# Performance work log

Hardware: AMD Instinct MI355X
Metric: run time of the kernel (lower is better)

The kernel has to match this reference:

```python
import jax, jax.numpy as jnp
import numpy as np

B, L, D, H = 2, 2048, 512, 8
HS = D // H          # head_size = 64
BLOCK = 2048         # block_size
EPS = 1e-5


def setup_inputs() -> dict:
    key = jax.random.key(0)
    ks = jax.random.split(key, 8)
    s = 0.02
    x = jax.random.normal(ks[0], (B, L, D), jnp.float32)
    mask = jnp.triu(jnp.ones((1, 1, L, L), bool), k=1)  # causal: True above diag
    wq = jax.random.normal(ks[1], (D, D), jnp.float32) * s
    wk = jax.random.normal(ks[2], (D, D), jnp.float32) * s
    wv = jax.random.normal(ks[3], (D, D), jnp.float32) * s
    wo = jax.random.normal(ks[4], (D, D), jnp.float32) * s
    Er = jax.random.normal(ks[5], (H, BLOCK, HS), jnp.float32)
    bq = jnp.zeros((D,), jnp.float32)
    bk = jnp.zeros((D,), jnp.float32)
    bv = jnp.zeros((D,), jnp.float32)
    bo = jnp.zeros((D,), jnp.float32)
    ln_g = jnp.ones((D,), jnp.float32)
    ln_b = jnp.zeros((D,), jnp.float32)
    return dict(x=x, mask=mask, ln_g=ln_g, ln_b=ln_b, wq=wq, bq=bq,
                wk=wk, bk=bk, wv=wv, bv=bv, wo=wo, bo=bo, Er=Er)


def _skew(qe):
    # qe: [B, H, L, L] -> pad last dim on the left, reshape trick, drop first row
    padded = jnp.pad(qe, ((0, 0), (0, 0), (0, 0), (1, 0)))
    b, h, l, l1 = padded.shape
    return padded.reshape(b, h, l1, l)[:, :, 1:, :]


def reference(x, mask, ln_g, ln_b, wq, bq, wk, bk, wv, bv, wo, bo, Er):
    l = x.shape[1]
    # LayerNorm
    mu = jnp.mean(x, axis=-1, keepdims=True)
    var = jnp.mean((x - mu) ** 2, axis=-1, keepdims=True)
    hn = (x - mu) / jnp.sqrt(var + EPS) * ln_g + ln_b
    # QKV: [B, H, L, HS]
    q = (hn @ wq.T + bq).reshape(-1, l, H, HS).transpose(0, 2, 1, 3)
    k = (hn @ wk.T + bk).reshape(-1, l, H, HS).transpose(0, 2, 1, 3)
    v = (hn @ wv.T + bv).reshape(-1, l, H, HS).transpose(0, 2, 1, 3)
    # relative position bias via skew
    Ers = Er[:, BLOCK - l:, :]                       # [H, l, HS]
    QEr = jnp.einsum('bhld,hmd->bhlm', q, Ers)       # [B, H, L, L]
    SRel = _skew(QEr)
    # scaled dot-product scores
    w = jnp.einsum('bhld,bhmd->bhlm', q, k) * (HS ** -0.5)
    w = jnp.where(mask, -jnp.inf, w)
    SRel = jnp.where(mask, -jnp.inf, SRel)
    w = jax.nn.softmax(w + SRel, axis=-1)            # dropout omitted (eval mode)
    out = jnp.einsum('bhlm,bhmd->bhld', w, v)
    out = out.transpose(0, 2, 1, 3).reshape(-1, l, D)
    return out @ wo.T + bo
```

## Files before the change

kernel.cpp:

```cpp
#include <hip/hip_runtime.h>

#define LSEQ 2048
#define DIM 512
#define NH 8
#define HS 64

typedef __attribute__((ext_vector_type(8))) short short8;
typedef __attribute__((ext_vector_type(4))) float f32x4;

__device__ inline unsigned short f2bf(float f) {
  union { float f; unsigned u; } a; a.f = f;
  unsigned r = a.u + 0x7FFFu + ((a.u >> 16) & 1u);
  return (unsigned short)(r >> 16);
}
__device__ inline float bf2f(unsigned short h) {
  union { unsigned u; float f; } a; a.u = ((unsigned)h) << 16;
  return a.f;
}
__device__ inline unsigned cvtpk(float lo, float hi) {
  unsigned r;
  asm("v_cvt_pk_bf16_f32 %0, %1, %2" : "=v"(r) : "v"(lo), "v"(hi));
  return r;
}

__device__ inline f32x4 mfma_bf16(short8 a, short8 b, f32x4 c) {
  return __builtin_amdgcn_mfma_f32_16x16x32_bf16(a, b, c, 0, 0, 0);
}

__device__ inline short8 ld8(const unsigned short* p) {
  return *reinterpret_cast<const short8*>(p);
}

#define GLLDS(SRC, DST) __builtin_amdgcn_global_load_lds( \
    (const __attribute__((address_space(1))) void*)(SRC), \
    (__attribute__((address_space(3))) void*)(DST), 16, 0, 0)

__device__ inline int frag_idx(int row, int d) {
  return (((row >> 4) * 2 + (d >> 5)) << 9) + (((row & 15) + ((d >> 3) & 3) * 16) << 3) + (d & 7);
}

__global__ __launch_bounds__(256) void cvt_all_kernel(
    const float* __restrict__ wq, const float* __restrict__ wk,
    const float* __restrict__ wv, const float* __restrict__ wo,
    const float* __restrict__ Er,
    unsigned short* __restrict__ wqb, unsigned short* __restrict__ wkb,
    unsigned short* __restrict__ wvb, unsigned short* __restrict__ wob,
    unsigned short* __restrict__ erb) {
  int b = blockIdx.x;
  if (b < 1024) {
    const float* src; unsigned short* dst; int off;
    if (b < 256)       { src = wq; dst = wqb; off = b; }
    else if (b < 512)  { src = wk; dst = wkb; off = b - 256; }
    else if (b < 768)  { src = wv; dst = wvb; off = b - 512; }
    else               { src = wo; dst = wob; off = b - 768; }
    int i = (off * 256 + threadIdx.x) * 4;
    float4 v = *reinterpret_cast<const float4*>(src + i);
    unsigned lo = (unsigned)f2bf(v.x) | ((unsigned)f2bf(v.y) << 16);
    unsigned hi = (unsigned)f2bf(v.z) | ((unsigned)f2bf(v.w) << 16);
    uint2 pk; pk.x = lo; pk.y = hi;
    *reinterpret_cast<uint2*>(dst + i) = pk;
  } else {
    const float scl = 1.4426950408889634f;
    int i = ((b - 1024) * 256 + threadIdx.x) * 4;
    int hh = i >> 17;
    int rem = i & ((1 << 17) - 1);
    int er = rem >> 6, d = rem & 63;
    float4 v = *reinterpret_cast<const float4*>(Er + i);
    unsigned lo = (unsigned)f2bf(v.x * scl) | ((unsigned)f2bf(v.y * scl) << 16);
    unsigned hi = (unsigned)f2bf(v.z * scl) | ((unsigned)f2bf(v.w * scl) << 16);
    uint2 pk; pk.x = lo; pk.y = hi;
    unsigned short* dst = erb + (size_t)hh * LSEQ * HS + frag_idx(er, d);
    *reinterpret_cast<uint2*>(dst) = pk;
  }
}

__global__ __launch_bounds__(256) void ln_kernel(const float* __restrict__ x,
    const float* __restrict__ g, const float* __restrict__ bta,
    unsigned short* __restrict__ hn) {
  int lane = threadIdx.x & 63, w = threadIdx.x >> 6;
  int row = blockIdx.x * 4 + w;
  const float4* xr = reinterpret_cast<const float4*>(x + (size_t)row * DIM);
  float4 a = xr[2 * lane], c = xr[2 * lane + 1];
  float s = a.x + a.y + a.z + a.w + c.x + c.y + c.z + c.w;
  float sq = a.x * a.x + a.y * a.y + a.z * a.z + a.w * a.w +
             c.x * c.x + c.y * c.y + c.z * c.z + c.w * c.w;
#pragma unroll
  for (int off = 1; off < 64; off <<= 1) {
    s += __shfl_xor(s, off);
    sq += __shfl_xor(sq, off);
  }
  float mu = s * (1.f / DIM);
  float var = sq * (1.f / DIM) - mu * mu;
  float rstd = rsqrtf(var + 1e-5f);
  float4 g0 = reinterpret_cast<const float4*>(g)[2 * lane];
  float4 g1 = reinterpret_cast<const float4*>(g)[2 * lane + 1];
  float4 b0 = reinterpret_cast<const float4*>(bta)[2 * lane];
  float4 b1 = reinterpret_cast<const float4*>(bta)[2 * lane + 1];
  uint4 o;
  o.x = (unsigned)f2bf((a.x - mu) * rstd * g0.x + b0.x) |
        ((unsigned)f2bf((a.y - mu) * rstd * g0.y + b0.y) << 16);
  o.y = (unsigned)f2bf((a.z - mu) * rstd * g0.z + b0.z) |
        ((unsigned)f2bf((a.w - mu) * rstd * g0.w + b0.w) << 16);
  o.z = (unsigned)f2bf((c.x - mu) * rstd * g1.x + b1.x) |
        ((unsigned)f2bf((c.y - mu) * rstd * g1.y + b1.y) << 16);
  o.w = (unsigned)f2bf((c.z - mu) * rstd * g1.z + b1.z) |
        ((unsigned)f2bf((c.w - mu) * rstd * g1.w + b1.w) << 16);
  reinterpret_cast<uint4*>(hn)[(size_t)row * 64 + lane] = o;
}

__global__ __launch_bounds__(256, 3) void qkv_kernel(const unsigned short* __restrict__ hn,
    const unsigned short* __restrict__ wqb, const unsigned short* __restrict__ wkb,
    const unsigned short* __restrict__ wvb,
    const float* __restrict__ bq, const float* __restrict__ bk, const float* __restrict__ bv,
    unsigned short* __restrict__ qo, unsigned short* __restrict__ ko,
    unsigned short* __restrict__ vT) {
  __shared__ unsigned short As[3][128 * 32];
  __shared__ unsigned short Bs[3][128 * 32];
  int tid = threadIdx.x, lane = tid & 63, w = tid >> 6;
  int mcol = lane & 15, grp = lane >> 4;
  int l4 = lane >> 2, lql = lane & 3;
  int bid = blockIdx.x;
  int mat = bid >> 7;
  int rem = bid & 127;
  int m0 = (rem >> 2) << 7;
  int n0 = (rem & 3) << 7;
  const unsigned short* W = (mat == 0) ? wqb : (mat == 1) ? wkb : wvb;
  const float* bias = (mat == 0) ? bq : (mat == 1) ? bk : bv;
  float scl = (mat == 1) ? 0.18033688011112042f : 1.f;
  int wr = w >> 1, wc = w & 1;

  f32x4 acc[4][4];
#pragma unroll
  for (int i = 0; i < 4; ++i)
#pragma unroll
    for (int j = 0; j < 4; ++j) acc[i][j] = (f32x4){0.f, 0.f, 0.f, 0.f};

#pragma unroll
  for (int j = 0; j < 2; ++j) {
    int row = 32 * w + 16 * j + l4;
    GLLDS(hn + (size_t)(m0 + row) * DIM + lql * 8, &As[0][(32 * w + 16 * j) * 32]);
    GLLDS(W + (size_t)(n0 + row) * DIM + lql * 8, &Bs[0][(32 * w + 16 * j) * 32]);
  }
  for (int kk = 0; kk < 16; ++kk) {
    int buf = kk % 3;
    if (kk < 15) {
      int nbuf = (kk + 1) % 3;
      int k0 = (kk + 1) * 32;
#pragma unroll
      for (int j = 0; j < 2; ++j) {
        int row = 32 * w + 16 * j + l4;
        GLLDS(hn + (size_t)(m0 + row) * DIM + k0 + lql * 8, &As[nbuf][(32 * w + 16 * j) * 32]);
        GLLDS(W + (size_t)(n0 + row) * DIM + k0 + lql * 8, &Bs[nbuf][(32 * w + 16 * j) * 32]);
      }
      asm volatile("s_waitcnt vmcnt(4)\n\ts_barrier" ::: "memory");
    } else {
      asm volatile("s_waitcnt vmcnt(0)\n\ts_barrier" ::: "memory");
    }
    const unsigned short* AL = As[buf];
    const unsigned short* BL = Bs[buf];
    short8 af[4], bf[4];
#pragma unroll
    for (int f = 0; f < 4; ++f) {
      af[f] = ld8(&AL[(wr * 64 + f * 16 + mcol) * 32 + grp * 8]);
      bf[f] = ld8(&BL[(wc * 64 + f * 16 + mcol) * 32 + grp * 8]);
    }
#pragma unroll
    for (int fi = 0; fi < 4; ++fi)
#pragma unroll
      for (int fj = 0; fj < 4; ++fj)
        acc[fi][fj] = mfma_bf16(af[fi], bf[fj], acc[fi][fj]);
  }
#pragma unroll
  for (int fj = 0; fj < 4; ++fj) {
    int n = n0 + wc * 64 + fj * 16 + mcol;
    int hh = n >> 6, d = n & 63;
    float bsv = bias[n];
#pragma unroll
    for (int fi = 0; fi < 4; ++fi) {
#pragma unroll
      for (int r = 0; r < 4; ++r) {
        int m = m0 + wr * 64 + fi * 16 + 4 * grp + r;
        float val = (acc[fi][fj][r] + bsv) * scl;
        int b = m >> 11, l = m & (LSEQ - 1);
        unsigned short hv = f2bf(val);
        size_t base = (size_t)(b * NH + hh) * HS * LSEQ;
        if (mat == 2) {
          int idx = (((l >> 5) * 4 + (d >> 4)) * 64 + ((l >> 3) & 3) * 16 + (d & 15)) * 8 + (l & 7);
          vT[base + idx] = hv;
        } else if (mat == 1) {
          ko[base + frag_idx(l, d)] = hv;
        } else {
          qo[((size_t)(b * NH + hh) * LSEQ + l) * HS + d] = hv;
        }
      }
    }
  }
}

__global__ __launch_bounds__(256, 3) void attn_kernel(const unsigned short* __restrict__ q,
    const unsigned short* __restrict__ k, const unsigned short* __restrict__ vT,
    const unsigned short* __restrict__ erb, char* __restrict__ partials) {
  __shared__ float Uall[4][16 * 84];
  int tid = threadIdx.x, lane = tid & 63, w = tid >> 6;
  int mcol = lane & 15, grp = lane >> 4;
  float* U = Uall[w];

  int bid = blockIdx.x;
  int xcd = bid & 7, s = bid >> 3;
  int hi2 = (s >= 80) ? 1 : 0;
  int bh = xcd + 8 * hi2;
  int ub = 79 - (s - 80 * hi2);
  int gp = (ub < 8) ? 0 : (ub < 24) ? 1 : (ub < 48) ? 2 : 3;
  int st0 = (gp == 0) ? 0 : (gp == 1) ? 8 : (gp == 2) ? 24 : 48;
  int idx = ub - st0;
  int tq = idx / (gp + 1);
  int cc = idx - tq * (gp + 1);
  int t64 = 8 * gp + tq;
  int qi0 = t64 << 6;
  int c0 = cc << 9;
  int kend = min(c0 + 512, qi0 + 64);
  int nkb = (kend - c0 + 63) >> 6;
  int h = bh & 7;

  const unsigned short* Qb = q + (size_t)bh * LSEQ * HS;
  const unsigned short* Kb = k + (size_t)bh * LSEQ * HS;
  const unsigned short* Vb = vT + (size_t)bh * HS * LSEQ;
  const unsigned short* Eb = erb + (size_t)h * LSEQ * HS;

  int qi0w = qi0 + 16 * w;
  short8 qf0 = ld8(Qb + (size_t)(qi0w + mcol) * HS + 8 * grp);
  short8 qf1 = ld8(Qb + (size_t)(qi0w + mcol) * HS + 32 + 8 * grp);

  f32x4 o[4];
#pragma unroll
  for (int i = 0; i < 4; ++i) o[i] = (f32x4){0.f, 0.f, 0.f, 0.f};
  float lacc = 0.f;
  int srcA = mcol | ((grp & 1) << 5);
  int srcB = srcA + 16;
  bool hi = (grp >= 2);
  int loff = lane * 8;

  for (int kb = 0; kb < nkb; ++kb) {
    int kj0 = c0 + (kb << 6);
    int E0w = 2032 - qi0w + kj0;
    short8 kf[8];
#pragma unroll
    for (int t = 0; t < 4; ++t) {
      int blk = ((kj0 >> 4) + t) * 2;
      kf[2 * t]     = ld8(Kb + (size_t)blk * 512 + loff);
      kf[2 * t + 1] = ld8(Kb + (size_t)(blk + 1) * 512 + loff);
    }
    short8 vf[8];
#pragma unroll
    for (int s2 = 0; s2 < 2; ++s2)
#pragma unroll
      for (int dt = 0; dt < 4; ++dt)
        vf[s2 * 4 + dt] = ld8(Vb + (size_t)(((kj0 >> 5) + s2) * 4 + dt) * 512 + loff);
#pragma unroll
    for (int jt = 0; jt < 5; ++jt) {
      int g = (E0w >> 4) + jt;
      if (g > 127) g = 127;
      short8 ef0 = ld8(Eb + (size_t)(g * 2) * 512 + loff);
      short8 ef1 = ld8(Eb + (size_t)(g * 2 + 1) * 512 + loff);
      f32x4 uu = (f32x4){0.f, 0.f, 0.f, 0.f};
      uu = mfma_bf16(ef0, qf0, uu);
      uu = mfma_bf16(ef1, qf1, uu);
      *reinterpret_cast<f32x4*>(&U[mcol * 84 + 16 * jt + 4 * grp]) = uu;
    }
    f32x4 stv[4];
#pragma unroll
    for (int t = 0; t < 4; ++t) {
      f32x4 a_ = (f32x4){0.f, 0.f, 0.f, 0.f};
      a_ = mfma_bf16(kf[2 * t], qf0, a_);
      a_ = mfma_bf16(kf[2 * t + 1], qf1, a_);
      stv[t] = a_;
    }
    float lt[4][4];
    bool anymask = (kj0 + 63) > qi0w;
    if (anymask) {
#pragma unroll
      for (int t = 0; t < 4; ++t) {
        const float* up = &U[mcol * 84 + 16 * t + 4 * grp - mcol + 15];
#pragma unroll
        for (int r = 0; r < 4; ++r) {
          int n = 16 * t + 4 * grp + r;
          float val = stv[t][r] + up[r];
          val = (kj0 + n > qi0w + mcol) ? -1e30f : val;
          float p_ = exp2f(val);
          lt[t][r] = p_;
          lacc += p_;
        }
      }
    } else {
#pragma unroll
      for (int t = 0; t < 4; ++t) {
        const float* up = &U[mcol * 84 + 16 * t + 4 * grp - mcol + 15];
#pragma unroll
        for (int r = 0; r < 4; ++r) {
          float p_ = exp2f(stv[t][r] + up[r]);
          lt[t][r] = p_;
          lacc += p_;
        }
      }
    }
    unsigned w0[4], w1[4];
#pragma unroll
    for (int t = 0; t < 4; ++t) {
      w0[t] = cvtpk(lt[t][0], lt[t][1]);
      w1[t] = cvtpk(lt[t][2], lt[t][3]);
    }
#pragma unroll
    for (int s2 = 0; s2 < 2; ++s2) {
      unsigned y0a = (unsigned)__shfl((int)w0[2 * s2], srcA);
      unsigned y0b = (unsigned)__shfl((int)w0[2 * s2 + 1], srcA);
      unsigned y1a = (unsigned)__shfl((int)w1[2 * s2], srcA);
      unsigned y1b = (unsigned)__shfl((int)w1[2 * s2 + 1], srcA);
      unsigned y2a = (unsigned)__shfl((int)w0[2 * s2], srcB);
      unsigned y2b = (unsigned)__shfl((int)w0[2 * s2 + 1], srcB);
      unsigned y3a = (unsigned)__shfl((int)w1[2 * s2], srcB);
      unsigned y3b = (unsigned)__shfl((int)w1[2 * s2 + 1], srcB);
      union { unsigned u4[4]; short8 s8; } pu;
      pu.u4[0] = hi ? y0b : y0a;
      pu.u4[1] = hi ? y1b : y1a;
      pu.u4[2] = hi ? y2b : y2a;
      pu.u4[3] = hi ? y3b : y3a;
#pragma unroll
      for (int dt = 0; dt < 4; ++dt)
        o[dt] = mfma_bf16(vf[s2 * 4 + dt], pu.s8, o[dt]);
    }
  }

  float lsum = lacc;
  lsum += __shfl_xor(lsum, 16);
  lsum += __shfl_xor(lsum, 32);

  int pid = bh * 320 + ub * 4 + w;
  char* pb = partials + (size_t)pid * 2176;
  unsigned* Ob = (unsigned*)pb;
#pragma unroll
  for (int dt = 0; dt < 4; ++dt) {
    Ob[mcol * 32 + dt * 8 + grp * 2]     = cvtpk(o[dt][0], o[dt][1]);
    Ob[mcol * 32 + dt * 8 + grp * 2 + 1] = cvtpk(o[dt][2], o[dt][3]);
  }
  if (grp == 0) {
    ((float*)(pb + 2112))[mcol] = lsum;
  }
}

__global__ __launch_bounds__(256) void merge_kernel(const char* __restrict__ partials,
    unsigned short* __restrict__ attT) {
  int lane = threadIdx.x & 63, widx = threadIdx.x >> 6;
  int bid = blockIdx.x;
  int xcd = bid & 7, q_ = bid >> 3;
  int hi2 = (q_ >= 32) ? 1 : 0;
  int bh = xcd + 8 * hi2;
  int i = (q_ - 32 * hi2) * 4 + widx;
  int t64 = i >> 2, w = i & 3;
  int gp = t64 >> 3, tq = t64 & 7;
  int st0 = (gp == 0) ? 0 : (gp == 1) ? 8 : (gp == 2) ? 24 : 48;
  int nch = gp + 1;
  int row = lane >> 2, d0 = (lane & 3) << 4;
  float acc[16];
#pragma unroll
  for (int j = 0; j < 16; ++j) acc[j] = 0.f;
  float lsum = 0.f;
  for (int c = 0; c < nch; ++c) {
    int pid = bh * 320 + (st0 + tq * nch + c) * 4 + w;
    const char* pb = partials + (size_t)pid * 2176;
    lsum += ((const float*)(pb + 2112))[row];
    short8 v0 = *reinterpret_cast<const short8*>(pb + row * 128 + d0 * 2);
    short8 v1 = *reinterpret_cast<const short8*>(pb + row * 128 + d0 * 2 + 16);
#pragma unroll
    for (int j = 0; j < 8; ++j) {
      acc[j]     += bf2f((unsigned short)v0[j]);
      acc[8 + j] += bf2f((unsigned short)v1[j]);
    }
  }
  float inv = 1.f / lsum;
  int b = bh >> 3, h = bh & 7;
  unsigned short* dst = attT + ((size_t)(b * LSEQ) + i * 16 + row) * DIM + h * HS + d0;
  union { unsigned short us[16]; short8 s8[2]; } ou;
#pragma unroll
  for (int j = 0; j < 16; ++j) ou.us[j] = f2bf(acc[j] * inv);
  *reinterpret_cast<short8*>(dst) = ou.s8[0];
  *reinterpret_cast<short8*>(dst + 8) = ou.s8[1];
}

__global__ __launch_bounds__(256, 3) void out_kernel(const unsigned short* __restrict__ attT,
    const unsigned short* __restrict__ wob, const float* __restrict__ bo,
    float* __restrict__ out) {
  __shared__ unsigned short As[3][128 * 32];
  __shared__ unsigned short Bs[3][64 * 32];
  int tid = threadIdx.x, lane = tid & 63, w = tid >> 6;
  int mcol = lane & 15, grp = lane >> 4;
  int l4 = lane >> 2, lql = lane & 3;
  int bid = blockIdx.x;
  int m0 = (bid >> 3) << 7;
  int n0 = (bid & 7) << 6;
  int wr = w >> 1, wc = w & 1;

  f32x4 acc[4][2];
#pragma unroll
  for (int i = 0; i < 4; ++i)
#pragma unroll
    for (int j = 0; j < 2; ++j) acc[i][j] = (f32x4){0.f, 0.f, 0.f, 0.f};

#pragma unroll
  for (int j = 0; j < 2; ++j) {
    int row = 32 * w + 16 * j + l4;
    GLLDS(attT + (size_t)(m0 + row) * DIM + lql * 8, &As[0][(32 * w + 16 * j) * 32]);
  }
  {
    int row = 16 * w + l4;
    GLLDS(wob + (size_t)(n0 + row) * DIM + lql * 8, &Bs[0][(16 * w) * 32]);
  }
  for (int kk = 0; kk < 16; ++kk) {
    int buf = kk % 3;
    if (kk < 15) {
      int nbuf = (kk + 1) % 3;
      int k0 = (kk + 1) * 32;
#pragma unroll
      for (int j = 0; j < 2; ++j) {
        int row = 32 * w + 16 * j + l4;
        GLLDS(attT + (size_t)(m0 + row) * DIM + k0 + lql * 8, &As[nbuf][(32 * w + 16 * j) * 32]);
      }
      {
        int row = 16 * w + l4;
        GLLDS(wob + (size_t)(n0 + row) * DIM + k0 + lql * 8, &Bs[nbuf][(16 * w) * 32]);
      }
      asm volatile("s_waitcnt vmcnt(3)\n\ts_barrier" ::: "memory");
    } else {
      asm volatile("s_waitcnt vmcnt(0)\n\ts_barrier" ::: "memory");
    }
    const unsigned short* AL = As[buf];
    const unsigned short* BL = Bs[buf];
    short8 af[4], bf[2];
#pragma unroll
    for (int f = 0; f < 4; ++f)
      af[f] = ld8(&AL[(wr * 64 + f * 16 + mcol) * 32 + grp * 8]);
#pragma unroll
    for (int f = 0; f < 2; ++f)
      bf[f] = ld8(&BL[(wc * 32 + f * 16 + mcol) * 32 + grp * 8]);
#pragma unroll
    for (int fi = 0; fi < 4; ++fi)
#pragma unroll
      for (int fj = 0; fj < 2; ++fj)
        acc[fi][fj] = mfma_bf16(af[fi], bf[fj], acc[fi][fj]);
  }
#pragma unroll
  for (int fj = 0; fj < 2; ++fj) {
    int n = n0 + wc * 32 + fj * 16 + mcol;
    float bsv = bo[n];
#pragma unroll
    for (int fi = 0; fi < 4; ++fi) {
#pragma unroll
      for (int r = 0; r < 4; ++r) {
        int m = m0 + wr * 64 + fi * 16 + 4 * grp + r;
        out[(size_t)m * DIM + n] = acc[fi][fj][r] + bsv;
      }
    }
  }
}

extern "C" void kernel_launch(void* const* d_in, const int* in_sizes, int n_in,
                              void* d_out, int out_size, void* d_ws, size_t ws_size,
                              hipStream_t stream) {
  const float* x    = (const float*)d_in[0];
  const float* ln_g = (const float*)d_in[2];
  const float* ln_b = (const float*)d_in[3];
  const float* wq   = (const float*)d_in[4];
  const float* bq   = (const float*)d_in[5];
  const float* wk   = (const float*)d_in[6];
  const float* bk   = (const float*)d_in[7];
  const float* wv   = (const float*)d_in[8];
  const float* bv   = (const float*)d_in[9];
  const float* wo   = (const float*)d_in[10];
  const float* bo   = (const float*)d_in[11];
  const float* Er   = (const float*)d_in[12];
  float* out = (float*)d_out;

  char* ws = (char*)d_ws;
  unsigned short* hn   = (unsigned short*)(ws);
  unsigned short* qb   = (unsigned short*)(ws + (4u << 20));
  unsigned short* kb   = (unsigned short*)(ws + (8u << 20));
  unsigned short* vT   = (unsigned short*)(ws + (12u << 20));
  unsigned short* erb  = (unsigned short*)(ws + (16u << 20));
  unsigned short* attT = (unsigned short*)(ws + (18u << 20));
  unsigned short* wqb  = (unsigned short*)(ws + (22u << 20));
  unsigned short* wkb  = wqb + 512 * 512;
  unsigned short* wvb  = wkb + 512 * 512;
  unsigned short* wob  = wvb + 512 * 512;
  char* partials       = ws + (24u << 20);

  cvt_all_kernel<<<2048, 256, 0, stream>>>(wq, wk, wv, wo, Er, wqb, wkb, wvb, wob, erb);
  ln_kernel<<<1024, 256, 0, stream>>>(x, ln_g, ln_b, hn);
  qkv_kernel<<<384, 256, 0, stream>>>(hn, wqb, wkb, wvb, bq, bk, bv, qb, kb, vT);
  attn_kernel<<<1280, 256, 0, stream>>>(qb, kb, vT, erb, partials);
  merge_kernel<<<512, 256, 0, stream>>>(partials, attT);
  out_kernel<<<256, 256, 0, stream>>>(attT, wob, bo, out);
}
```

Before: 83.45 us.

## Give each attention wave 32 query rows to reuse K, V and Er fragments

Each wave now owns two 16-row query groups (32 rows) instead of one, so the K, V and relative-position Er fragments it loads are reused across both groups. Work units become 32-row tiles per wave, which halves the attention grid and changes the partials layout and merge indexing to match. The exp2f call is replaced by the raw v_exp_f32 instruction. This costs more registers per wave (doubled accumulators and score tiles) and more LDS, which may lower occupancy, and the larger tiles give coarser load balance across the causal triangle.

Measured after the change: 76.57 us. -8.3%, faster.

```diff
diff --git a/kernel.cpp b/kernel.cpp
--- a/kernel.cpp
+++ b/kernel.cpp
@@ -20,6 +20,11 @@
 __device__ inline unsigned cvtpk(float lo, float hi) {
   unsigned r;
   asm("v_cvt_pk_bf16_f32 %0, %1, %2" : "=v"(r) : "v"(lo), "v"(hi));
+  return r;
+}
+__device__ inline float fexp2(float x) {
+  float r;
+  asm("v_exp_f32 %0, %1" : "=v"(r) : "v"(x));
   return r;
 }
 
@@ -200,25 +205,25 @@
 __global__ __launch_bounds__(256, 3) void attn_kernel(const unsigned short* __restrict__ q,
     const unsigned short* __restrict__ k, const unsigned short* __restrict__ vT,
     const unsigned short* __restrict__ erb, char* __restrict__ partials) {
-  __shared__ float Uall[4][16 * 84];
+  __shared__ float Uall[4][32 * 100];
   int tid = threadIdx.x, lane = tid & 63, w = tid >> 6;
   int mcol = lane & 15, grp = lane >> 4;
   float* U = Uall[w];
 
   int bid = blockIdx.x;
   int xcd = bid & 7, s = bid >> 3;
-  int hi2 = (s >= 80) ? 1 : 0;
+  int hi2 = (s >= 40) ? 1 : 0;
   int bh = xcd + 8 * hi2;
-  int ub = 79 - (s - 80 * hi2);
-  int gp = (ub < 8) ? 0 : (ub < 24) ? 1 : (ub < 48) ? 2 : 3;
-  int st0 = (gp == 0) ? 0 : (gp == 1) ? 8 : (gp == 2) ? 24 : 48;
-  int idx = ub - st0;
-  int tq = idx / (gp + 1);
-  int cc = idx - tq * (gp + 1);
-  int t64 = 8 * gp + tq;
-  int qi0 = t64 << 6;
+  int bu = s - 40 * hi2;
+  int ubp = 159 - (bu * 4 + w);
+  int T, cc;
+  if (ubp < 16)      { T = ubp; cc = 0; }
+  else if (ubp < 48) { int idx = ubp - 16; T = 16 + (idx >> 1); cc = idx & 1; }
+  else if (ubp < 96) { int idx = ubp - 48; int t3 = idx / 3; T = 32 + t3; cc = idx - 3 * t3; }
+  else               { int idx = ubp - 96; T = 48 + (idx >> 2); cc = idx & 3; }
+  int qi0w = T << 5;
   int c0 = cc << 9;
-  int kend = min(c0 + 512, qi0 + 64);
+  int kend = min(c0 + 512, qi0w + 32);
   int nkb = (kend - c0 + 63) >> 6;
   int h = bh & 7;
 
@@ -227,14 +232,19 @@
   const unsigned short* Vb = vT + (size_t)bh * HS * LSEQ;
   const unsigned short* Eb = erb + (size_t)h * LSEQ * HS;
 
-  int qi0w = qi0 + 16 * w;
-  short8 qf0 = ld8(Qb + (size_t)(qi0w + mcol) * HS + 8 * grp);
-  short8 qf1 = ld8(Qb + (size_t)(qi0w + mcol) * HS + 32 + 8 * grp);
-
-  f32x4 o[4];
-#pragma unroll
-  for (int i = 0; i < 4; ++i) o[i] = (f32x4){0.f, 0.f, 0.f, 0.f};
-  float lacc = 0.f;
+  short8 qf[2][2];
+#pragma unroll
+  for (int mg = 0; mg < 2; ++mg) {
+    qf[mg][0] = ld8(Qb + (size_t)(qi0w + 16 * mg + mcol) * HS + 8 * grp);
+    qf[mg][1] = ld8(Qb + (size_t)(qi0w + 16 * mg + mcol) * HS + 32 + 8 * grp);
+  }
+
+  f32x4 o[2][4];
+#pragma unroll
+  for (int mg = 0; mg < 2; ++mg)
+#pragma unroll
+    for (int i = 0; i < 4; ++i) o[mg][i] = (f32x4){0.f, 0.f, 0.f, 0.f};
+  float la0 = 0.f, la1 = 0.f;
   int srcA = mcol | ((grp & 1) << 5);
   int srcB = srcA + 16;
   bool hi = (grp >= 2);
@@ -242,7 +252,27 @@
 
   for (int kb = 0; kb < nkb; ++kb) {
     int kj0 = c0 + (kb << 6);
-    int E0w = 2032 - qi0w + kj0;
+    int E0 = 2016 - qi0w + kj0;
+    int g0 = E0 >> 4;
+    short8 ef[12];
+#pragma unroll
+    for (int jt = 0; jt < 6; ++jt) {
+      int gg = g0 + jt;
+      if (gg > 127) gg = 127;
+      ef[2 * jt]     = ld8(Eb + (size_t)(gg * 2) * 512 + loff);
+      ef[2 * jt + 1] = ld8(Eb + (size_t)(gg * 2 + 1) * 512 + loff);
+    }
+#pragma unroll
+    for (int jt = 0; jt < 6; ++jt) {
+      f32x4 u0 = (f32x4){0.f, 0.f, 0.f, 0.f};
+      u0 = mfma_bf16(ef[2 * jt], qf[0][0], u0);
+      u0 = mfma_bf16(ef[2 * jt + 1], qf[0][1], u0);
+      f32x4 u1 = (f32x4){0.f, 0.f, 0.f, 0.f};
+      u1 = mfma_bf16(ef[2 * jt], qf[1][0], u1);
+      u1 = mfma_bf16(ef[2 * jt + 1], qf[1][1], u1);
+      *reinterpret_cast<f32x4*>(&U[mcol * 100 + 16 * jt + 4 * grp]) = u0;
+      *reinterpret_cast<f32x4*>(&U[(mcol + 16) * 100 + 16 * jt + 4 * grp]) = u1;
+    }
     short8 kf[8];
 #pragma unroll
     for (int t = 0; t < 4; ++t) {
@@ -250,6 +280,48 @@
       kf[2 * t]     = ld8(Kb + (size_t)blk * 512 + loff);
       kf[2 * t + 1] = ld8(Kb + (size_t)(blk + 1) * 512 + loff);
     }
+    f32x4 stv[2][4];
+#pragma unroll
+    for (int mg = 0; mg < 2; ++mg)
+#pragma unroll
+      for (int t = 0; t < 4; ++t) {
+        f32x4 a_ = (f32x4){0.f, 0.f, 0.f, 0.f};
+        a_ = mfma_bf16(kf[2 * t], qf[mg][0], a_);
+        a_ = mfma_bf16(kf[2 * t + 1], qf[mg][1], a_);
+        stv[mg][t] = a_;
+      }
+    float lt[2][4][4];
+#pragma unroll
+    for (int mg = 0; mg < 2; ++mg) {
+      int m = mcol + 16 * mg;
+      bool am = (kj0 + 63) > (qi0w + 16 * mg);
+      if (am) {
+#pragma unroll
+        for (int t = 0; t < 4; ++t) {
+          const float* up = &U[m * 100 + 16 * t + 4 * grp - m + 31];
+#pragma unroll
+          for (int r = 0; r < 4; ++r) {
+            int n = 16 * t + 4 * grp + r;
+            float val = stv[mg][t][r] + up[r];
+            val = (kj0 + n > qi0w + m) ? -1e30f : val;
+            float p_ = fexp2(val);
+            lt[mg][t][r] = p_;
+            if (mg == 0) la0 += p_; else la1 += p_;
+          }
+        }
+      } else {
+#pragma unroll
+        for (int t = 0; t < 4; ++t) {
+          const float* up = &U[m * 100 + 16 * t + 4 * grp - m + 31];
+#pragma unroll
+          for (int r = 0; r < 4; ++r) {
+            float p_ = fexp2(stv[mg][t][r] + up[r]);
+            lt[mg][t][r] = p_;
+            if (mg == 0) la0 += p_; else la1 += p_;
+          }
+        }
+      }
+    }
     short8 vf[8];
 #pragma unroll
     for (int s2 = 0; s2 < 2; ++s2)
@@ -257,133 +329,94 @@
       for (int dt = 0; dt < 4; ++dt)
         vf[s2 * 4 + dt] = ld8(Vb + (size_t)(((kj0 >> 5) + s2) * 4 + dt) * 512 + loff);
 #pragma unroll
-    for (int jt = 0; jt < 5; ++jt) {
-      int g = (E0w >> 4) + jt;
-      if (g > 127) g = 127;
-      short8 ef0 = ld8(Eb + (size_t)(g * 2) * 512 + loff);
-      short8 ef1 = ld8(Eb + (size_t)(g * 2 + 1) * 512 + loff);
-      f32x4 uu = (f32x4){0.f, 0.f, 0.f, 0.f};
-      uu = mfma_bf16(ef0, qf0, uu);
-      uu = mfma_bf16(ef1, qf1, uu);
-      *reinterpret_cast<f32x4*>(&U[mcol * 84 + 16 * jt + 4 * grp]) = uu;
-    }
-    f32x4 stv[4];
-#pragma unroll
-    for (int t = 0; t < 4; ++t) {
-      f32x4 a_ = (f32x4){0.f, 0.f, 0.f, 0.f};
-      a_ = mfma_bf16(kf[2 * t], qf0, a_);
-      a_ = mfma_bf16(kf[2 * t + 1], qf1, a_);
-      stv[t] = a_;
-    }
-    float lt[4][4];
-    bool anymask = (kj0 + 63) > qi0w;
-    if (anymask) {
+    for (int mg = 0; mg < 2; ++mg) {
+      unsigned w0[4], w1[4];
 #pragma unroll
       for (int t = 0; t < 4; ++t) {
-        const float* up = &U[mcol * 84 + 16 * t + 4 * grp - mcol + 15];
-#pragma unroll
-        for (int r = 0; r < 4; ++r) {
-          int n = 16 * t + 4 * grp + r;
-          float val = stv[t][r] + up[r];
-          val = (kj0 + n > qi0w + mcol) ? -1e30f : val;
-          float p_ = exp2f(val);
-          lt[t][r] = p_;
-          lacc += p_;
-        }
-      }
-    } else {
-#pragma unroll
-      for (int t = 0; t < 4; ++t) {
-        const float* up = &U[mcol * 84 + 16 * t + 4 * grp - mcol + 15];
-#pragma unroll
-        for (int r = 0; r < 4; ++r) {
-          float p_ = exp2f(stv[t][r] + up[r]);
-          lt[t][r] = p_;
-          lacc += p_;
-        }
-      }
-    }
-    unsigned w0[4], w1[4];
-#pragma unroll
-    for (int t = 0; t < 4; ++t) {
-      w0[t] = cvtpk(lt[t][0], lt[t][1]);
-      w1[t] = cvtpk(lt[t][2], lt[t][3]);
-    }
-#pragma unroll
-    for (int s2 = 0; s2 < 2; ++s2) {
-      unsigned y0a = (unsigned)__shfl((int)w0[2 * s2], srcA);
-      unsigned y0b = (unsigned)__shfl((int)w0[2 * s2 + 1], srcA);
-      unsigned y1a = (unsigned)__shfl((int)w1[2 * s2], srcA);
-      unsigned y1b = (unsigned)__shfl((int)w1[2 * s2 + 1], srcA);
-      unsigned y2a = (unsigned)__shfl((int)w0[2 * s2], srcB);
-      unsigned y2b = (unsigned)__shfl((int)w0[2 * s2 + 1], srcB);
-      unsigned y3a = (unsigned)__shfl((int)w1[2 * s2], srcB);
-      unsigned y3b = (unsigned)__shfl((int)w1[2 * s2 + 1], srcB);
-      union { unsigned u4[4]; short8 s8; } pu;
-      pu.u4[0] = hi ? y0b : y0a;
-      pu.u4[1] = hi ? y1b : y1a;
-      pu.u4[2] = hi ? y2b : y2a;
-      pu.u4[3] = hi ? y3b : y3a;
-#pragma unroll
-      for (int dt = 0; dt < 4; ++dt)
-        o[dt] = mfma_bf16(vf[s2 * 4 + dt], pu.s8, o[dt]);
-    }
-  }
-
-  float lsum = lacc;
-  lsum += __shfl_xor(lsum, 16);
-  lsum += __shfl_xor(lsum, 32);
-
-  int pid = bh * 320 + ub * 4 + w;
-  char* pb = partials + (size_t)pid * 2176;
+        w0[t] = cvtpk(lt[mg][t][0], lt[mg][t][1]);
+        w1[t] = cvtpk(lt[mg][t][2], lt[mg][t][3]);
+      }
+#pragma unroll
+      for (int s2 = 0; s2 < 2; ++s2) {
+        unsigned y0a = (unsigned)__shfl((int)w0[2 * s2], srcA);
+        unsigned y0b = (unsigned)__shfl((int)w0[2 * s2 + 1], srcA);
+        unsigned y1a = (unsigned)__shfl((int)w1[2 * s2], srcA);
+        unsigned y1b = (unsigned)__shfl((int)w1[2 * s2 + 1], srcA);
+        unsigned y2a = (unsigned)__shfl((int)w0[2 * s2], srcB);
+        unsigned y2b = (unsigned)__shfl((int)w0[2 * s2 + 1], srcB);
+        unsigned y3a = (unsigned)__shfl((int)w1[2 * s2], srcB);
+        unsigned y3b = (unsigned)__shfl((int)w1[2 * s2 + 1], srcB);
+        union { unsigned u4[4]; short8 s8; } pu;
+        pu.u4[0] = hi ? y0b : y0a;
+        pu.u4[1] = hi ? y1b : y1a;
+        pu.u4[2] = hi ? y2b : y2a;
+        pu.u4[3] = hi ? y3b : y3a;
+#pragma unroll
+        for (int dt = 0; dt < 4; ++dt)
+          o[mg][dt] = mfma_bf16(vf[s2 * 4 + dt], pu.s8, o[mg][dt]);
+      }
+    }
+  }
+
+  la0 += __shfl_xor(la0, 16);
+  la0 += __shfl_xor(la0, 32);
+  la1 += __shfl_xor(la1, 16);
+  la1 += __shfl_xor(la1, 32);
+
+  int pid = bh * 160 + ubp;
+  char* pb = partials + (size_t)pid * 4224;
   unsigned* Ob = (unsigned*)pb;
 #pragma unroll
-  for (int dt = 0; dt < 4; ++dt) {
-    Ob[mcol * 32 + dt * 8 + grp * 2]     = cvtpk(o[dt][0], o[dt][1]);
-    Ob[mcol * 32 + dt * 8 + grp * 2 + 1] = cvtpk(o[dt][2], o[dt][3]);
-  }
+  for (int mg = 0; mg < 2; ++mg)
+#pragma unroll
+    for (int dt = 0; dt < 4; ++dt) {
+      Ob[(mcol + 16 * mg) * 32 + dt * 8 + grp * 2]     = cvtpk(o[mg][dt][0], o[mg][dt][1]);
+      Ob[(mcol + 16 * mg) * 32 + dt * 8 + grp * 2 + 1] = cvtpk(o[mg][dt][2], o[mg][dt][3]);
+    }
   if (grp == 0) {
-    ((float*)(pb + 2112))[mcol] = lsum;
+    ((float*)(pb + 4096))[mcol]      = la0;
+    ((float*)(pb + 4096))[mcol + 16] = la1;
   }
 }
 
 __global__ __launch_bounds__(256) void merge_kernel(const char* __restrict__ partials,
     unsigned short* __restrict__ attT) {
-  int lane = threadIdx.x & 63, widx = threadIdx.x >> 6;
+  int lane = threadIdx.x & 63, w = threadIdx.x >> 6;
   int bid = blockIdx.x;
-  int xcd = bid & 7, q_ = bid >> 3;
-  int hi2 = (q_ >= 32) ? 1 : 0;
+  int xcd = bid & 7, s = bid >> 3;
+  int hi2 = (s >= 16) ? 1 : 0;
   int bh = xcd + 8 * hi2;
-  int i = (q_ - 32 * hi2) * 4 + widx;
-  int t64 = i >> 2, w = i & 3;
-  int gp = t64 >> 3, tq = t64 & 7;
-  int st0 = (gp == 0) ? 0 : (gp == 1) ? 8 : (gp == 2) ? 24 : 48;
-  int nch = gp + 1;
-  int row = lane >> 2, d0 = (lane & 3) << 4;
-  float acc[16];
-#pragma unroll
-  for (int j = 0; j < 16; ++j) acc[j] = 0.f;
+  int T = (s - 16 * hi2) * 4 + w;
+  int g = T >> 4;
+  int start = (g == 0) ? 0 : (g == 1) ? 16 : (g == 2) ? 48 : 96;
+  int nch = g + 1;
+  int base_u = bh * 160 + start + (T & 15) * nch;
+  int row = lane & 31, dh = lane >> 5;
+  float acc[32];
+#pragma unroll
+  for (int j = 0; j < 32; ++j) acc[j] = 0.f;
   float lsum = 0.f;
   for (int c = 0; c < nch; ++c) {
-    int pid = bh * 320 + (st0 + tq * nch + c) * 4 + w;
-    const char* pb = partials + (size_t)pid * 2176;
-    lsum += ((const float*)(pb + 2112))[row];
-    short8 v0 = *reinterpret_cast<const short8*>(pb + row * 128 + d0 * 2);
-    short8 v1 = *reinterpret_cast<const short8*>(pb + row * 128 + d0 * 2 + 16);
-#pragma unroll
-    for (int j = 0; j < 8; ++j) {
-      acc[j]     += bf2f((unsigned short)v0[j]);
-      acc[8 + j] += bf2f((unsigned short)v1[j]);
+    const char* pb = partials + (size_t)(base_u + c) * 4224;
+    lsum += ((const float*)(pb + 4096))[row];
+    const unsigned short* Op = (const unsigned short*)pb + row * 64 + dh * 32;
+#pragma unroll
+    for (int jj = 0; jj < 4; ++jj) {
+      short8 v = ld8(Op + jj * 8);
+#pragma unroll
+      for (int e = 0; e < 8; ++e)
+        acc[jj * 8 + e] += bf2f((unsigned short)v[e]);
     }
   }
   float inv = 1.f / lsum;
   int b = bh >> 3, h = bh & 7;
-  unsigned short* dst = attT + ((size_t)(b * LSEQ) + i * 16 + row) * DIM + h * HS + d0;
-  union { unsigned short us[16]; short8 s8[2]; } ou;
-#pragma unroll
-  for (int j = 0; j < 16; ++j) ou.us[j] = f2bf(acc[j] * inv);
-  *reinterpret_cast<short8*>(dst) = ou.s8[0];
-  *reinterpret_cast<short8*>(dst + 8) = ou.s8[1];
+  unsigned short* dst = attT + ((size_t)(b * LSEQ) + T * 32 + row) * DIM + h * HS + dh * 32;
+  union { unsigned short us[32]; short8 s8[4]; } ou;
+#pragma unroll
+  for (int j = 0; j < 32; ++j) ou.us[j] = f2bf(acc[j] * inv);
+#pragma unroll
+  for (int jj = 0; jj < 4; ++jj)
+    *reinterpret_cast<short8*>(dst + jj * 8) = ou.s8[jj];
 }
 
 __global__ __launch_bounds__(256, 3) void out_kernel(const unsigned short* __restrict__ attT,
@@ -495,7 +528,7 @@
   cvt_all_kernel<<<2048, 256, 0, stream>>>(wq, wk, wv, wo, Er, wqb, wkb, wvb, wob, erb);
   ln_kernel<<<1024, 256, 0, stream>>>(x, ln_g, ln_b, hn);
   qkv_kernel<<<384, 256, 0, stream>>>(hn, wqb, wkb, wvb, bq, bk, bv, qb, kb, vT);
-  attn_kernel<<<1280, 256, 0, stream>>>(qb, kb, vT, erb, partials);
-  merge_kernel<<<512, 256, 0, stream>>>(partials, attT);
+  attn_kernel<<<640, 256, 0, stream>>>(qb, kb, vT, erb, partials);
+  merge_kernel<<<256, 256, 0, stream>>>(partials, attT);
   out_kernel<<<256, 256, 0, stream>>>(attT, wob, bo, out);
 }
```
